# Optimization experiments

Measured on AMD Instinct MI355X. Metric: run time of the kernel, lower is better.

The kernel has to match this reference:

```python
import jax, jax.numpy as jnp
import numpy as np

B, S, E = 256, 512, 1024   # batch, src_len, encoder hidden (== decoder hidden)
H = 1024                   # decoder hidden
AV = 1024                  # att_vec_size
A, TY = 128, 128           # action_embed_size, type_embed_size
T = 48                     # max_sketch_num (decode steps)
NP_, NT_ = 97, 20          # len(prod2id), len(type2id)
IN = A + AV + TY           # LSTMCell input dim = 1280


def setup_inputs() -> dict:
    key = jax.random.key(0)
    ks = jax.random.split(key, 16)
    s = 0.02
    return {
        "encoder_outputs": jax.random.normal(ks[0], (B, S, E), jnp.float32),
        "action_ids": jax.random.randint(ks[1], (T, B), 0, NP_, jnp.int32),
        "type_ids": jax.random.randint(ks[2], (T, B), 0, NT_, jnp.int32),
        "W_ih": jax.random.normal(ks[3], (4 * H, IN), jnp.float32) * s,
        "b_ih": jax.random.normal(ks[4], (4 * H,), jnp.float32) * s,
        "W_hh": jax.random.normal(ks[5], (4 * H, H), jnp.float32) * s,
        "b_hh": jax.random.normal(ks[6], (4 * H,), jnp.float32) * s,
        "W_att": jax.random.normal(ks[7], (H, E), jnp.float32) * s,
        "W_av": jax.random.normal(ks[8], (AV, 2 * H), jnp.float32) * s,
        "W_qa": jax.random.normal(ks[9], (A, AV), jnp.float32) * s,
        "b_qa": jax.random.normal(ks[10], (A,), jnp.float32) * s,
        "prod_embed": jax.random.normal(ks[11], (NP_, A), jnp.float32) * s,
        "prod_bias": jnp.zeros((NP_,), jnp.float32),
        "type_embed_tab": jax.random.normal(ks[12], (NT_, TY), jnp.float32) * s,
        "W_init": jax.random.normal(ks[13], (H, E), jnp.float32) * s,
        "b_init": jax.random.normal(ks[14], (H,), jnp.float32) * s,
    }


def reference(encoder_outputs, action_ids, type_ids, W_ih, b_ih, W_hh, b_hh,
              W_att, W_av, W_qa, b_qa, prod_embed, prod_bias, type_embed_tab,
              W_init, b_init):
    # dropout in eval mode -> identity; src_encodings == encoder_outputs
    src = encoder_outputs                              # [B,S,E]
    src_lin = jnp.einsum('bse,he->bsh', src, W_att)    # att_sketch_linear (no bias)

    # init_decoder_state: adaptive_max_pool1d over sequence, tanh(linear), c0 = 0
    pooled = src.max(axis=1)                           # [B,E]
    h0 = jnp.tanh(pooled @ W_init.T + b_init)          # [B,H]
    c0 = jnp.zeros_like(h0)
    att0 = jnp.zeros((src.shape[0], W_av.shape[0]), src.dtype)

    # previous-action / previous-type embeddings; step 0 uses all-zero input x
    a_prev = prod_embed[action_ids]                    # [T,B,A]
    ty_prev = type_embed_tab[type_ids]                 # [T,B,TY]
    m = (jnp.arange(a_prev.shape[0]) > 0).astype(src.dtype)[:, None, None]  # [T,1,1]
    a_prev = a_prev * m
    ty_prev = ty_prev * m

    def step(carry, xs):
        h, c, att_tm1 = carry
        a_e, ty_e, mt = xs
        x = jnp.concatenate([a_e, att_tm1 * mt, ty_e], axis=-1)  # [B,IN]
        # PyTorch LSTMCell gate order: i, f, g, o
        gates = x @ W_ih.T + b_ih + h @ W_hh.T + b_hh            # [B,4H]
        i, f, g, o = jnp.split(gates, 4, axis=-1)
        c_t = jax.nn.sigmoid(f) * c + jax.nn.sigmoid(i) * jnp.tanh(g)
        h_t = jax.nn.sigmoid(o) * jnp.tanh(c_t)
        # dot-product attention over projected utterance encodings
        scores = jnp.einsum('bsh,bh->bs', src_lin, h_t)
        w = jax.nn.softmax(scores, axis=-1)
        ctx = jnp.einsum('bs,bse->be', w, src)
        att_t = jnp.tanh(jnp.concatenate([h_t, ctx], axis=-1) @ W_av.T)  # [B,AV]
        # production_readout: tanh(linear) then tied production-embedding output layer
        q = jnp.tanh(att_t @ W_qa.T + b_qa)                      # [B,A]
        probs = jax.nn.softmax(q @ prod_embed.T + prod_bias, axis=-1)  # [B,NP]
        return (h_t, c_t, att_t), probs

    _, probs = jax.lax.scan(step, (h0, c0, att0), (a_prev, ty_prev, m))
    return probs  # [T,B,n_prods]
```

## Files before the change

kernel.cpp:

```cpp
#include <hip/hip_runtime.h>


typedef short s16x8 __attribute__((ext_vector_type(8)));
typedef float f32x4 __attribute__((ext_vector_type(4)));

__device__ __forceinline__ unsigned short f2b(float x) {
  unsigned int u = __float_as_uint(x);
  return (unsigned short)((u + 0x7fffu + ((u >> 16) & 1u)) >> 16);
}
__device__ __forceinline__ float b2f(unsigned short h) {
  return __uint_as_float(((unsigned int)h) << 16);
}
__device__ __forceinline__ float sigm(float x) { return 1.f / (1.f + __expf(-x)); }


template <int WRITE_B16>
__global__ __launch_bounds__(256) void pool_convert(const float* __restrict__ src,
                                                    unsigned short* __restrict__ srcb,
                                                    unsigned short* __restrict__ pooledb) {
  int b = blockIdx.x >> 2;
  int e = (blockIdx.x & 3) * 256 + threadIdx.x;
  const float* p = src + (size_t)b * 524288 + e;
  float m = -3e38f;
  for (int s = 0; s < 512; s += 8) {
    float v[8];
#pragma unroll
    for (int i = 0; i < 8; ++i) v[i] = __builtin_nontemporal_load(p + (size_t)(s + i) * 1024);
#pragma unroll
    for (int i = 0; i < 8; ++i) {
      m = fmaxf(m, v[i]);
      if (WRITE_B16) srcb[(size_t)b * 524288 + (size_t)(s + i) * 1024 + e] = f2b(v[i]);
    }
  }
  pooledb[b * 1024 + e] = f2b(m);
}

__global__ __launch_bounds__(256) void conv_wcat(const float* __restrict__ wih,
                                                 const float* __restrict__ whh,
                                                 unsigned short* __restrict__ wcat) {
  int idx = blockIdx.x * 256 + threadIdx.x;
  int np = idx / 2304;
  int k = idx - np * 2304;
  int j = np >> 2, g = np & 3;
  int n = g * 1024 + j;
  float v;
  if (k < 1024) v = wih[n * 1280 + 128 + k];
  else if (k < 2048) v = whh[n * 1024 + (k - 1024)];
  else if (k < 2176) v = wih[n * 1280 + (k - 2048)];
  else v = wih[n * 1280 + 1152 + (k - 2176)];
  wcat[idx] = f2b(v);
}

__global__ __launch_bounds__(256) void conv_bsum(const float* __restrict__ bih,
                                                 const float* __restrict__ bhh,
                                                 float* __restrict__ bsum) {
  int idx = blockIdx.x * 256 + threadIdx.x;
  int j = idx >> 2, g = idx & 3;
  int n = g * 1024 + j;
  bsum[idx] = bih[n] + bhh[n];
}

__global__ __launch_bounds__(256) void conv_wattT(const float* __restrict__ watt,
                                                  unsigned short* __restrict__ wt) {
  int idx = blockIdx.x * 256 + threadIdx.x;
  int e = idx >> 10, h = idx & 1023;
  wt[idx] = f2b(watt[h * 1024 + e]);
}

__global__ __launch_bounds__(256) void conv_f2b(const float* __restrict__ s,
                                                unsigned short* __restrict__ d, int n) {
  int idx = blockIdx.x * 256 + threadIdx.x;
  if (idx < n) d[idx] = f2b(s[idx]);
}

__global__ __launch_bounds__(256) void conv_wqaT(const float* __restrict__ wqa,
                                                 float* __restrict__ wt) {
  int idx = blockIdx.x * 256 + threadIdx.x;
  int k = idx >> 7, j = idx & 127;
  wt[idx] = wqa[j * 1024 + k];
}

__global__ __launch_bounds__(256) void conv_xaty(const int* __restrict__ action,
                                                 const int* __restrict__ type_ids,
                                                 const float* __restrict__ prod_emb,
                                                 const float* __restrict__ type_emb,
                                                 unsigned short* __restrict__ xaty) {
  int idx = blockIdx.x * 256 + threadIdx.x;
  int t = idx >> 16;
  int b = (idx >> 8) & 255;
  int kk = idx & 255;
  float v = 0.f;
  if (t > 0) {
    if (kk < 128) v = prod_emb[action[t * 256 + b] * 128 + kk];
    else v = type_emb[type_ids[t * 256 + b] * 128 + (kk - 128)];
  }
  xaty[idx] = f2b(v);
}

__global__ __launch_bounds__(256) void init0(unsigned short* __restrict__ xs0,
                                             float* __restrict__ c) {
  int idx = blockIdx.x * 256 + threadIdx.x;
  int b = idx >> 10, e = idx & 1023;
  xs0[(size_t)b * 2048 + e] = 0;
  c[idx] = 0.f;
}

template <int EPI, int K>
__global__ __launch_bounds__(256) void gemm_bt(const unsigned short* __restrict__ A, int lda,
                                               const unsigned short* __restrict__ B, int ldb,
                                               float* __restrict__ C, int ldc,
                                               const float* __restrict__ bias,
                                               unsigned short* __restrict__ aux, int aux_ld,
                                               int aux_off) {
  int lane = threadIdx.x & 63;
  int wid = threadIdx.x >> 6;
  int mw = blockIdx.y * 64 + (wid >> 1) * 32;
  int nw = blockIdx.x * 64 + (wid & 1) * 32;
  int lr = lane & 15;
  int kg = lane >> 4;
  const unsigned short* a0p = A + (size_t)(mw + lr) * lda + kg * 8;
  const unsigned short* a1p = a0p + (size_t)16 * lda;
  const unsigned short* b0p = B + (size_t)(nw + lr) * ldb + kg * 8;
  const unsigned short* b1p = b0p + (size_t)16 * ldb;
  f32x4 acc00 = {0.f, 0.f, 0.f, 0.f};
  f32x4 acc01 = acc00, acc10 = acc00, acc11 = acc00;
#pragma unroll 4
  for (int k = 0; k < K; k += 32) {
    s16x8 a0 = *(const s16x8*)(a0p + k);
    s16x8 a1 = *(const s16x8*)(a1p + k);
    s16x8 b0 = *(const s16x8*)(b0p + k);
    s16x8 b1 = *(const s16x8*)(b1p + k);
    acc00 = __builtin_amdgcn_mfma_f32_16x16x32_bf16(a0, b0, acc00, 0, 0, 0);
    acc01 = __builtin_amdgcn_mfma_f32_16x16x32_bf16(a0, b1, acc01, 0, 0, 0);
    acc10 = __builtin_amdgcn_mfma_f32_16x16x32_bf16(a1, b0, acc10, 0, 0, 0);
    acc11 = __builtin_amdgcn_mfma_f32_16x16x32_bf16(a1, b1, acc11, 0, 0, 0);
  }
  int r0 = mw + kg * 4;
  int c0 = nw + lr;
#pragma unroll
  for (int fi = 0; fi < 2; ++fi) {
#pragma unroll
    for (int fj = 0; fj < 2; ++fj) {
      f32x4 acc = (fi == 0) ? (fj == 0 ? acc00 : acc01) : (fj == 0 ? acc10 : acc11);
      int rr = r0 + fi * 16;
      int cc = c0 + fj * 16;
#pragma unroll
      for (int r = 0; r < 4; ++r) {
        float v = acc[r];
        if constexpr (EPI == 2) v = tanhf(v + bias[cc]);
        if constexpr (EPI == 1) v = tanhf(v);
        if constexpr (EPI != 0) aux[(size_t)(rr + r) * aux_ld + aux_off + cc] = f2b(v);
        if constexpr (EPI != 2) C[(size_t)(rr + r) * ldc + cc] = v;
      }
    }
  }
}

template <int EPI, int K>
__global__ __launch_bounds__(256) void gemm32(const unsigned short* __restrict__ A, int lda,
                                              const unsigned short* __restrict__ B, int ldb,
                                              float* __restrict__ C, int ldc,
                                              unsigned short* __restrict__ aux, int aux_ld,
                                              int aux_off) {
  int lane = threadIdx.x & 63;
  int wid = threadIdx.x >> 6;
  int mw = blockIdx.y * 32 + (wid >> 1) * 16;
  int nw = blockIdx.x * 32 + (wid & 1) * 16;
  int lr = lane & 15;
  int kg = lane >> 4;
  const unsigned short* ap = A + (size_t)(mw + lr) * lda + kg * 8;
  const unsigned short* bp = B + (size_t)(nw + lr) * ldb + kg * 8;
  f32x4 acc = {0.f, 0.f, 0.f, 0.f};
#pragma unroll 8
  for (int k = 0; k < K; k += 32) {
    s16x8 a = *(const s16x8*)(ap + k);
    s16x8 b = *(const s16x8*)(bp + k);
    acc = __builtin_amdgcn_mfma_f32_16x16x32_bf16(a, b, acc, 0, 0, 0);
  }
  int rr = mw + kg * 4;
  int cc = nw + lr;
#pragma unroll
  for (int r = 0; r < 4; ++r) {
    float v = acc[r];
    if constexpr (EPI == 1) {
      v = tanhf(v);
      aux[(size_t)(rr + r) * aux_ld + aux_off + cc] = f2b(v);
    }
    C[(size_t)(rr + r) * ldc + cc] = v;
  }
}

__global__ __launch_bounds__(256) void gates_fused(const unsigned short* __restrict__ xin,
                                                   const unsigned short* __restrict__ xaty,
                                                   const unsigned short* __restrict__ wcat,
                                                   const float* __restrict__ bsum,
                                                   float* __restrict__ cbuf,
                                                   unsigned short* __restrict__ xout,
                                                   unsigned short* __restrict__ a2,
                                                   const float* __restrict__ attf,
                                                   const float* __restrict__ wqaT,
                                                   const float* __restrict__ b_qa,
                                                   const float* __restrict__ prod_emb,
                                                   const float* __restrict__ prod_bias,
                                                   float* __restrict__ out, int t) {
  __shared__ float ld[64][68];
  __shared__ float s_att[2][1024];
  __shared__ float s_q2[2][128];
  __shared__ float s_log[2][100];
  __shared__ float s_red[2][2];

  if (blockIdx.y == 4) {
    if (t == 0) return;
    int half = threadIdx.x >> 7;
    int ltid = threadIdx.x & 127;
#pragma unroll
    for (int rep = 0; rep < 2; ++rep) {
      int b = blockIdx.x * 4 + rep * 2 + half;
      const float* ap = attf + (size_t)b * 1024;
      for (int i = ltid; i < 1024; i += 128) s_att[half][i] = ap[i];
      __syncthreads();
      float acc = b_qa[ltid];
      for (int k = 0; k < 1024; ++k) acc += s_att[half][k] * wqaT[k * 128 + ltid];
      s_q2[half][ltid] = tanhf(acc);
      __syncthreads();
      if (ltid < 97) {
        float a = prod_bias[ltid];
        const float* pe = prod_emb + ltid * 128;
        float aa = 0.f;
        for (int k = 0; k < 128; ++k) aa += s_q2[half][k] * pe[k];
        s_log[half][ltid] = a + aa;
      }
      __syncthreads();
      if (ltid == 0) {
        float M = s_log[half][0];
        for (int k2 = 1; k2 < 97; ++k2) M = fmaxf(M, s_log[half][k2]);
        float D = 0.f;
        for (int k2 = 0; k2 < 97; ++k2) D += __expf(s_log[half][k2] - M);
        s_red[half][0] = M;
        s_red[half][1] = D;
      }
      __syncthreads();
      if (ltid < 97)
        out[((size_t)(t - 1) * 256 + b) * 97 + ltid] =
            __expf(s_log[half][ltid] - s_red[half][0]) / s_red[half][1];
      __syncthreads();
    }
    return;
  }

  int lane = threadIdx.x & 63;
  int wid = threadIdx.x >> 6;
  int mwl = (wid >> 1) * 32;
  int nwl = (wid & 1) * 32;
  int mw = blockIdx.y * 64 + mwl;
  int nw = blockIdx.x * 64 + nwl;
  int lr = lane & 15;
  int kg = lane >> 4;
  const unsigned short* a0p = xin + (size_t)(mw + lr) * 2048 + kg * 8;
  const unsigned short* a1p = a0p + (size_t)16 * 2048;
  const unsigned short* b0p = wcat + (size_t)(nw + lr) * 2304 + kg * 8;
  const unsigned short* b1p = b0p + (size_t)16 * 2304;
  f32x4 acc00 = {0.f, 0.f, 0.f, 0.f};
  f32x4 acc01 = acc00, acc10 = acc00, acc11 = acc00;
#pragma unroll 8
  for (int k = 0; k < 2048; k += 32) {
    s16x8 a0 = *(const s16x8*)(a0p + k);
    s16x8 a1 = *(const s16x8*)(a1p + k);
    s16x8 b0 = *(const s16x8*)(b0p + k);
    s16x8 b1 = *(const s16x8*)(b1p + k);
    acc00 = __builtin_amdgcn_mfma_f32_16x16x32_bf16(a0, b0, acc00, 0, 0, 0);
    acc01 = __builtin_amdgcn_mfma_f32_16x16x32_bf16(a0, b1, acc01, 0, 0, 0);
    acc10 = __builtin_amdgcn_mfma_f32_16x16x32_bf16(a1, b0, acc10, 0, 0, 0);
    acc11 = __builtin_amdgcn_mfma_f32_16x16x32_bf16(a1, b1, acc11, 0, 0, 0);
  }
  const unsigned short* c0p = xaty + (size_t)(mw + lr) * 256 + kg * 8;
  const unsigned short* c1p = c0p + (size_t)16 * 256;
#pragma unroll
  for (int k = 0; k < 256; k += 32) {
    s16x8 a0 = *(const s16x8*)(c0p + k);
    s16x8 a1 = *(const s16x8*)(c1p + k);
    s16x8 b0 = *(const s16x8*)(b0p + 2048 + k);
    s16x8 b1 = *(const s16x8*)(b1p + 2048 + k);
    acc00 = __builtin_amdgcn_mfma_f32_16x16x32_bf16(a0, b0, acc00, 0, 0, 0);
    acc01 = __builtin_amdgcn_mfma_f32_16x16x32_bf16(a0, b1, acc01, 0, 0, 0);
    acc10 = __builtin_amdgcn_mfma_f32_16x16x32_bf16(a1, b0, acc10, 0, 0, 0);
    acc11 = __builtin_amdgcn_mfma_f32_16x16x32_bf16(a1, b1, acc11, 0, 0, 0);
  }
  int r0 = mwl + kg * 4;
  int c0 = nwl + lr;
#pragma unroll
  for (int fi = 0; fi < 2; ++fi)
#pragma unroll
    for (int fj = 0; fj < 2; ++fj) {
      f32x4 acc = (fi == 0) ? (fj == 0 ? acc00 : acc01) : (fj == 0 ? acc10 : acc11);
#pragma unroll
      for (int r = 0; r < 4; ++r) ld[r0 + fi * 16 + r][c0 + fj * 16] = acc[r];
    }
  __syncthreads();
  int row = threadIdx.x >> 2;
  int col0 = (threadIdx.x & 3) * 16;
  int b = blockIdx.y * 64 + row;
  int jbase = blockIdx.x * 16 + (threadIdx.x & 3) * 4;
  float4 cold = *(const float4*)(cbuf + (size_t)b * 1024 + jbase);
  float cn[4];
  unsigned short hb[4];
#pragma unroll
  for (int i = 0; i < 4; ++i) {
    float4 bs = *(const float4*)(bsum + (size_t)(jbase + i) * 4);
    float vi = ld[row][col0 + 4 * i + 0] + bs.x;
    float vf = ld[row][col0 + 4 * i + 1] + bs.y;
    float vg = ld[row][col0 + 4 * i + 2] + bs.z;
    float vo = ld[row][col0 + 4 * i + 3] + bs.w;
    float co = (i == 0) ? cold.x : (i == 1) ? cold.y : (i == 2) ? cold.z : cold.w;
    float ct = sigm(vf) * co + sigm(vi) * tanhf(vg);
    float ht = sigm(vo) * tanhf(ct);
    cn[i] = ct;
    hb[i] = f2b(ht);
  }
  *(float4*)(cbuf + (size_t)b * 1024 + jbase) = make_float4(cn[0], cn[1], cn[2], cn[3]);
  ushort4 h4 = make_ushort4(hb[0], hb[1], hb[2], hb[3]);
  *(ushort4*)(xout + (size_t)b * 2048 + 1024 + jbase) = h4;
  *(ushort4*)(a2 + (size_t)b * 2048 + jbase) = h4;
}

template <int BF16P>
__global__ __launch_bounds__(1024) void flash_attn(const unsigned short* __restrict__ srcb,
                                                   const float* __restrict__ srcf,
                                                   const float* __restrict__ q,
                                                   unsigned short* __restrict__ a2) {
  __shared__ unsigned short lctx[16][1024];
  __shared__ float lm[16], ldn[16], lsc[16];
  __shared__ float sDinv;
  int b = blockIdx.x;
  int wid = threadIdx.x >> 6, lane = threadIdx.x & 63;
  float qr[16];
  {
    const float4* qp = (const float4*)(q + (size_t)b * 1024 + lane * 16);
#pragma unroll
    for (int i = 0; i < 4; ++i) {
      float4 t = qp[i];
      qr[4 * i] = t.x; qr[4 * i + 1] = t.y; qr[4 * i + 2] = t.z; qr[4 * i + 3] = t.w;
    }
  }
  float m = -3e38f, d = 0.f;
  float ctx[16];
#pragma unroll
  for (int i = 0; i < 16; ++i) ctx[i] = 0.f;
  int s0 = wid * 32;

  if (BF16P) {
    const unsigned short* rb = srcb + (size_t)b * 524288 + lane * 16;
    s16x8 u0 = __builtin_nontemporal_load((const s16x8*)(rb + (size_t)s0 * 1024));
    s16x8 u1 = __builtin_nontemporal_load((const s16x8*)(rb + (size_t)s0 * 1024 + 8));
    for (int s = 0; s < 32; ++s) {
      int rn = s0 + s + 1;
      rn = rn > 511 ? 511 : rn;
      s16x8 n0 = __builtin_nontemporal_load((const s16x8*)(rb + (size_t)rn * 1024));
      s16x8 n1 = __builtin_nontemporal_load((const s16x8*)(rb + (size_t)rn * 1024 + 8));
      float v[16];
#pragma unroll
      for (int i = 0; i < 8; ++i) {
        v[i] = b2f((unsigned short)u0[i]);
        v[8 + i] = b2f((unsigned short)u1[i]);
      }
      float sc = 0.f;
#pragma unroll
      for (int i = 0; i < 16; ++i) sc += v[i] * qr[i];
#pragma unroll
      for (int off = 1; off < 64; off <<= 1) sc += __shfl_xor(sc, off);
      float mn = fmaxf(m, sc);
      float scale = __expf(m - mn);
      float wgt = __expf(sc - mn);
      d = d * scale + wgt;
#pragma unroll
      for (int i = 0; i < 16; ++i) ctx[i] = ctx[i] * scale + wgt * v[i];
      m = mn;
      u0 = n0; u1 = n1;
    }
  } else {
    const float* rb = srcf + (size_t)b * 524288 + lane * 16;
    for (int s = 0; s < 32; ++s) {
      int r = s0 + s;
      float v[16];
#pragma unroll
      for (int i = 0; i < 4; ++i) {
        f32x4 t = __builtin_nontemporal_load((const f32x4*)(rb + (size_t)r * 1024 + 4 * i));
        v[4 * i] = t[0]; v[4 * i + 1] = t[1]; v[4 * i + 2] = t[2]; v[4 * i + 3] = t[3];
      }
      float sc = 0.f;
#pragma unroll
      for (int i = 0; i < 16; ++i) sc += v[i] * qr[i];
#pragma unroll
      for (int off = 1; off < 64; off <<= 1) sc += __shfl_xor(sc, off);
      float mn = fmaxf(m, sc);
      float scale = __expf(m - mn);
      float wgt = __expf(sc - mn);
      d = d * scale + wgt;
#pragma unroll
      for (int i = 0; i < 16; ++i) ctx[i] = ctx[i] * scale + wgt * v[i];
      m = mn;
    }
  }

#pragma unroll
  for (int i = 0; i < 16; ++i) lctx[wid][lane * 16 + i] = f2b(ctx[i]);
  if (lane == 0) { lm[wid] = m; ldn[wid] = d; }
  __syncthreads();
  if (threadIdx.x == 0) {
    float M = lm[0];
    for (int w2 = 1; w2 < 16; ++w2) M = fmaxf(M, lm[w2]);
    float D = 0.f;
    for (int w2 = 0; w2 < 16; ++w2) {
      float sc = __expf(lm[w2] - M);
      lsc[w2] = sc;
      D += sc * ldn[w2];
    }
    sDinv = 1.f / D;
  }
  __syncthreads();
  int e = threadIdx.x;
  float acc = 0.f;
#pragma unroll
  for (int w2 = 0; w2 < 16; ++w2) acc += lsc[w2] * b2f(lctx[w2][e]);
  a2[(size_t)b * 2048 + 1024 + e] = f2b(acc * sDinv);
}

__global__ __launch_bounds__(128) void readout(const float* __restrict__ att,
                                               const float* __restrict__ wqaT,
                                               const float* __restrict__ b_qa,
                                               const float* __restrict__ prod_emb,
                                               const float* __restrict__ prod_bias,
                                               float* __restrict__ out, int t) {
  __shared__ float s_att[1024], s_q2[128], s_log[97], s_red[2];
  int b = blockIdx.x;
  int tid = threadIdx.x;
  for (int i = tid; i < 1024; i += 128) s_att[i] = att[(size_t)b * 1024 + i];
  __syncthreads();
  float acc = b_qa[tid];
  for (int k = 0; k < 1024; ++k) acc += s_att[k] * wqaT[k * 128 + tid];
  s_q2[tid] = tanhf(acc);
  __syncthreads();
  if (tid < 97) {
    float a = prod_bias[tid];
    const float* pe = prod_emb + tid * 128;
    for (int k = 0; k < 128; ++k) a += s_q2[k] * pe[k];
    s_log[tid] = a;
  }
  __syncthreads();
  if (tid == 0) {
    float M = s_log[0];
    for (int k = 1; k < 97; ++k) M = fmaxf(M, s_log[k]);
    float D = 0.f;
    for (int k = 0; k < 97; ++k) D += __expf(s_log[k] - M);
    s_red[0] = M;
    s_red[1] = D;
  }
  __syncthreads();
  if (tid < 97)
    out[((size_t)t * 256 + b) * 97 + tid] = __expf(s_log[tid] - s_red[0]) / s_red[1];
}


extern "C" void kernel_launch(void* const* d_in, const int* in_sizes, int n_in,
                              void* d_out, int out_size, void* d_ws, size_t ws_size,
                              hipStream_t stream) {
  const float* src = (const float*)d_in[0];
  const int* action = (const int*)d_in[1];
  const int* type_ids = (const int*)d_in[2];
  const float* W_ih = (const float*)d_in[3];
  const float* b_ih = (const float*)d_in[4];
  const float* W_hh = (const float*)d_in[5];
  const float* b_hh = (const float*)d_in[6];
  const float* W_att = (const float*)d_in[7];
  const float* W_av = (const float*)d_in[8];
  const float* W_qa = (const float*)d_in[9];
  const float* b_qa = (const float*)d_in[10];
  const float* prod_emb = (const float*)d_in[11];
  const float* prod_bias = (const float*)d_in[12];
  const float* type_emb = (const float*)d_in[13];
  const float* W_init = (const float*)d_in[14];
  const float* b_init = (const float*)d_in[15];
  float* out = (float*)d_out;

  const size_t NEED_SMALL = 40910848ull;
  const size_t NEED_BIG = 309346304ull;
  bool big = ws_size >= NEED_BIG;
  if (!big && ws_size < NEED_SMALL) return;

  char* w = (char*)d_ws;
  size_t o = 0;
  unsigned short* wcat = (unsigned short*)(w + o); o += 18874368ull;
  unsigned short* wattT = (unsigned short*)(w + o); o += 2097152ull;
  unsigned short* wav = (unsigned short*)(w + o); o += 4194304ull;
  float* wqaT = (float*)(w + o); o += 524288ull;
  unsigned short* xaty = (unsigned short*)(w + o); o += 6291456ull;
  unsigned short* xstate0 = (unsigned short*)(w + o); o += 1048576ull;
  unsigned short* xstate1 = (unsigned short*)(w + o); o += 1048576ull;
  unsigned short* a2 = (unsigned short*)(w + o); o += 1048576ull;
  float* cbuf = (float*)(w + o); o += 1048576ull;
  float* qbuf = (float*)(w + o); o += 1048576ull;
  float* attf = (float*)(w + o); o += 1048576ull;
  unsigned short* pooledb = (unsigned short*)(w + o); o += 524288ull;
  unsigned short* winitb = (unsigned short*)(w + o); o += 2097152ull;
  float* bsum = (float*)(w + o); o += 16384ull;
  unsigned short* srcb = nullptr;
  if (big) { srcb = (unsigned short*)(w + o); o += 268435456ull; }

  if (big) pool_convert<1><<<1024, 256, 0, stream>>>(src, srcb, pooledb);
  else     pool_convert<0><<<1024, 256, 0, stream>>>(src, nullptr, pooledb);
  conv_wcat<<<36864, 256, 0, stream>>>(W_ih, W_hh, wcat);
  conv_bsum<<<16, 256, 0, stream>>>(b_ih, b_hh, bsum);
  conv_wattT<<<4096, 256, 0, stream>>>(W_att, wattT);
  conv_f2b<<<8192, 256, 0, stream>>>(W_av, wav, 2097152);
  conv_f2b<<<4096, 256, 0, stream>>>(W_init, winitb, 1048576);
  conv_wqaT<<<512, 256, 0, stream>>>(W_qa, wqaT);
  conv_xaty<<<12288, 256, 0, stream>>>(action, type_ids, prod_emb, type_emb, xaty);
  init0<<<1024, 256, 0, stream>>>(xstate0, cbuf);
  gemm_bt<2, 1024><<<dim3(16, 4), 256, 0, stream>>>(pooledb, 1024, winitb, 1024,
                                                    nullptr, 0, b_init, xstate0, 2048, 1024);

  for (int t = 0; t < 48; ++t) {
    const unsigned short* xin = (t & 1) ? xstate1 : xstate0;
    unsigned short* xout = (t & 1) ? xstate0 : xstate1;
    gates_fused<<<dim3(64, 5), 256, 0, stream>>>(xin, xaty + (size_t)t * 65536, wcat, bsum,
                                                 cbuf, xout, a2, attf, wqaT, b_qa, prod_emb,
                                                 prod_bias, out, t);
    gemm32<0, 1024><<<dim3(32, 8), 256, 0, stream>>>(a2, 2048, wattT, 1024, qbuf, 1024,
                                                     nullptr, 0, 0);
    if (big) flash_attn<1><<<256, 1024, 0, stream>>>(srcb, nullptr, qbuf, a2);
    else     flash_attn<0><<<256, 1024, 0, stream>>>(nullptr, src, qbuf, a2);
    gemm32<1, 2048><<<dim3(32, 8), 256, 0, stream>>>(a2, 2048, wav, 2048, attf, 1024,
                                                     xout, 2048, 0);
  }
  readout<<<256, 128, 0, stream>>>(attf, wqaT, b_qa, prod_emb, prod_bias, out, 47);
}
```

Before: 6.821 ms.

## Fuse query projection into flash attention and keep half of bf16 src cache-resident

Folds the per-step h·W_att query projection into the attention kernel, so each block computes its own 1024-wide query from h and the transposed W_att. This removes one GEMM launch and the qbuf round trip. The attention block shrinks to 512 threads, each wave streaming 64 rows. The first half of the bf16 source rows is now written and read with normal (temporal) accesses so it can stay in the MI355X's large last-level cache across the 48 steps, while the second half stays non-temporal. The cost is that every one of the 256 blocks re-reads the full 2 MB W_att with a scalar per-thread dot product, and there are fewer waves to hide latency.

```diff
diff --git a/kernel.cpp b/kernel.cpp
--- a/kernel.cpp
+++ b/kernel.cpp
@@ -12,6 +12,17 @@
   return __uint_as_float(((unsigned int)h) << 16);
 }
 __device__ __forceinline__ float sigm(float x) { return 1.f / (1.f + __expf(-x)); }
+
+template <int NT>
+__device__ __forceinline__ s16x8 ld8(const s16x8* p) {
+  if constexpr (NT) return __builtin_nontemporal_load(p);
+  else return *p;
+}
+template <int NT>
+__device__ __forceinline__ f32x4 ld4f(const f32x4* p) {
+  if constexpr (NT) return __builtin_nontemporal_load(p);
+  else return *p;
+}
 
 
 template <int WRITE_B16>
@@ -29,7 +40,12 @@
 #pragma unroll
     for (int i = 0; i < 8; ++i) {
       m = fmaxf(m, v[i]);
-      if (WRITE_B16) srcb[(size_t)b * 524288 + (size_t)(s + i) * 1024 + e] = f2b(v[i]);
+      if (WRITE_B16) {
+        unsigned short bv = f2b(v[i]);
+        unsigned short* dst = srcb + (size_t)b * 524288 + (size_t)(s + i) * 1024 + e;
+        if (s + i < 256) *dst = bv;
+        else __builtin_nontemporal_store(bv, dst);
+      }
     }
   }
   pooledb[b * 1024 + e] = f2b(m);
@@ -323,106 +339,148 @@
   *(ushort4*)(a2 + (size_t)b * 2048 + jbase) = h4;
 }
 
+template <int NT>
+__device__ __forceinline__ void stream_bf16(const unsigned short* rb, int s0,
+                                            const float* qr, float& m, float& d,
+                                            float* ctx) {
+  s16x8 c0 = ld8<NT>((const s16x8*)(rb + (size_t)s0 * 1024));
+  s16x8 c1 = ld8<NT>((const s16x8*)(rb + (size_t)s0 * 1024 + 8));
+  s16x8 d0 = ld8<NT>((const s16x8*)(rb + (size_t)(s0 + 1) * 1024));
+  s16x8 d1 = ld8<NT>((const s16x8*)(rb + (size_t)(s0 + 1) * 1024 + 8));
+  for (int s = 0; s < 64; ++s) {
+    int rn = s0 + s + 2;
+    rn = rn > 511 ? 511 : rn;
+    s16x8 e0 = ld8<NT>((const s16x8*)(rb + (size_t)rn * 1024));
+    s16x8 e1 = ld8<NT>((const s16x8*)(rb + (size_t)rn * 1024 + 8));
+    float v[16];
+#pragma unroll
+    for (int i = 0; i < 8; ++i) {
+      v[i] = b2f((unsigned short)c0[i]);
+      v[8 + i] = b2f((unsigned short)c1[i]);
+    }
+    float sc = 0.f;
+#pragma unroll
+    for (int i = 0; i < 16; ++i) sc += v[i] * qr[i];
+#pragma unroll
+    for (int off = 1; off < 64; off <<= 1) sc += __shfl_xor(sc, off);
+    float mn = fmaxf(m, sc);
+    float scale = __expf(m - mn);
+    float wgt = __expf(sc - mn);
+    d = d * scale + wgt;
+#pragma unroll
+    for (int i = 0; i < 16; ++i) ctx[i] = ctx[i] * scale + wgt * v[i];
+    m = mn;
+    c0 = d0; c1 = d1; d0 = e0; d1 = e1;
+  }
+}
+
+template <int NT>
+__device__ __forceinline__ void stream_f32(const float* rf, int s0, const float* qr,
+                                           float& m, float& d, float* ctx) {
+  for (int s = 0; s < 64; ++s) {
+    int rr = s0 + s;
+    float v[16];
+#pragma unroll
+    for (int i = 0; i < 4; ++i) {
+      f32x4 tq = ld4f<NT>((const f32x4*)(rf + (size_t)rr * 1024 + 4 * i));
+      v[4 * i] = tq[0]; v[4 * i + 1] = tq[1]; v[4 * i + 2] = tq[2]; v[4 * i + 3] = tq[3];
+    }
+    float sc = 0.f;
+#pragma unroll
+    for (int i = 0; i < 16; ++i) sc += v[i] * qr[i];
+#pragma unroll
+    for (int off = 1; off < 64; off <<= 1) sc += __shfl_xor(sc, off);
+    float mn = fmaxf(m, sc);
+    float scale = __expf(m - mn);
+    float wgt = __expf(sc - mn);
+    d = d * scale + wgt;
+#pragma unroll
+    for (int i = 0; i < 16; ++i) ctx[i] = ctx[i] * scale + wgt * v[i];
+    m = mn;
+  }
+}
+
 template <int BF16P>
-__global__ __launch_bounds__(1024) void flash_attn(const unsigned short* __restrict__ srcb,
-                                                   const float* __restrict__ srcf,
-                                                   const float* __restrict__ q,
-                                                   unsigned short* __restrict__ a2) {
-  __shared__ unsigned short lctx[16][1024];
-  __shared__ float lm[16], ldn[16], lsc[16];
-  __shared__ float sDinv;
-  int b = blockIdx.x;
-  int wid = threadIdx.x >> 6, lane = threadIdx.x & 63;
+__global__ __launch_bounds__(512) void flashq(const unsigned short* __restrict__ srcb,
+                                              const float* __restrict__ srcf,
+                                              const unsigned short* __restrict__ wattT,
+                                              unsigned short* __restrict__ a2) {
+  union SMem {
+    struct { float q[1024]; unsigned short h[1024]; } p;
+    struct { unsigned short lctx[8][1024]; float lm[8], ldn[8], lsc[8], sDinv; } c;
+  };
+  __shared__ SMem sm;
+  const int tid = threadIdx.x;
+  const int lane = tid & 63;
+  const int wv = tid >> 6;
+  const int b = blockIdx.x;
+  const int s0 = wv * 64;
+
+  sm.p.h[tid] = a2[(size_t)b * 2048 + tid];
+  sm.p.h[tid + 512] = a2[(size_t)b * 2048 + tid + 512];
+  __syncthreads();
+  {
+    const unsigned short* w0 = wattT + (size_t)(2 * tid) * 1024;
+    const unsigned short* w1 = w0 + 1024;
+    float acc0 = 0.f, acc1 = 0.f;
+    for (int k = 0; k < 1024; k += 8) {
+      s16x8 hv = *(const s16x8*)(sm.p.h + k);
+      s16x8 wa = *(const s16x8*)(w0 + k);
+      s16x8 wb = *(const s16x8*)(w1 + k);
+#pragma unroll
+      for (int i = 0; i < 8; ++i) {
+        float hf = b2f((unsigned short)hv[i]);
+        acc0 += hf * b2f((unsigned short)wa[i]);
+        acc1 += hf * b2f((unsigned short)wb[i]);
+      }
+    }
+    sm.p.q[2 * tid] = acc0;
+    sm.p.q[2 * tid + 1] = acc1;
+  }
+  __syncthreads();
   float qr[16];
-  {
-    const float4* qp = (const float4*)(q + (size_t)b * 1024 + lane * 16);
-#pragma unroll
-    for (int i = 0; i < 4; ++i) {
-      float4 t = qp[i];
-      qr[4 * i] = t.x; qr[4 * i + 1] = t.y; qr[4 * i + 2] = t.z; qr[4 * i + 3] = t.w;
-    }
-  }
+#pragma unroll
+  for (int i = 0; i < 16; ++i) qr[i] = sm.p.q[lane * 16 + i];
+  __syncthreads();
+
   float m = -3e38f, d = 0.f;
   float ctx[16];
 #pragma unroll
   for (int i = 0; i < 16; ++i) ctx[i] = 0.f;
-  int s0 = wid * 32;
-
   if (BF16P) {
     const unsigned short* rb = srcb + (size_t)b * 524288 + lane * 16;
-    s16x8 u0 = __builtin_nontemporal_load((const s16x8*)(rb + (size_t)s0 * 1024));
-    s16x8 u1 = __builtin_nontemporal_load((const s16x8*)(rb + (size_t)s0 * 1024 + 8));
-    for (int s = 0; s < 32; ++s) {
-      int rn = s0 + s + 1;
-      rn = rn > 511 ? 511 : rn;
-      s16x8 n0 = __builtin_nontemporal_load((const s16x8*)(rb + (size_t)rn * 1024));
-      s16x8 n1 = __builtin_nontemporal_load((const s16x8*)(rb + (size_t)rn * 1024 + 8));
-      float v[16];
-#pragma unroll
-      for (int i = 0; i < 8; ++i) {
-        v[i] = b2f((unsigned short)u0[i]);
-        v[8 + i] = b2f((unsigned short)u1[i]);
-      }
-      float sc = 0.f;
-#pragma unroll
-      for (int i = 0; i < 16; ++i) sc += v[i] * qr[i];
-#pragma unroll
-      for (int off = 1; off < 64; off <<= 1) sc += __shfl_xor(sc, off);
-      float mn = fmaxf(m, sc);
-      float scale = __expf(m - mn);
-      float wgt = __expf(sc - mn);
-      d = d * scale + wgt;
-#pragma unroll
-      for (int i = 0; i < 16; ++i) ctx[i] = ctx[i] * scale + wgt * v[i];
-      m = mn;
-      u0 = n0; u1 = n1;
-    }
+    if (wv < 4) stream_bf16<0>(rb, s0, qr, m, d, ctx);
+    else        stream_bf16<1>(rb, s0, qr, m, d, ctx);
   } else {
-    const float* rb = srcf + (size_t)b * 524288 + lane * 16;
-    for (int s = 0; s < 32; ++s) {
-      int r = s0 + s;
-      float v[16];
-#pragma unroll
-      for (int i = 0; i < 4; ++i) {
-        f32x4 t = __builtin_nontemporal_load((const f32x4*)(rb + (size_t)r * 1024 + 4 * i));
-        v[4 * i] = t[0]; v[4 * i + 1] = t[1]; v[4 * i + 2] = t[2]; v[4 * i + 3] = t[3];
-      }
-      float sc = 0.f;
-#pragma unroll
-      for (int i = 0; i < 16; ++i) sc += v[i] * qr[i];
-#pragma unroll
-      for (int off = 1; off < 64; off <<= 1) sc += __shfl_xor(sc, off);
-      float mn = fmaxf(m, sc);
-      float scale = __expf(m - mn);
-      float wgt = __expf(sc - mn);
-      d = d * scale + wgt;
-#pragma unroll
-      for (int i = 0; i < 16; ++i) ctx[i] = ctx[i] * scale + wgt * v[i];
-      m = mn;
-    }
-  }
-
-#pragma unroll
-  for (int i = 0; i < 16; ++i) lctx[wid][lane * 16 + i] = f2b(ctx[i]);
-  if (lane == 0) { lm[wid] = m; ldn[wid] = d; }
-  __syncthreads();
-  if (threadIdx.x == 0) {
-    float M = lm[0];
-    for (int w2 = 1; w2 < 16; ++w2) M = fmaxf(M, lm[w2]);
+    const float* rf = srcf + (size_t)b * 524288 + lane * 16;
+    if (wv < 4) stream_f32<0>(rf, s0, qr, m, d, ctx);
+    else        stream_f32<1>(rf, s0, qr, m, d, ctx);
+  }
+
+#pragma unroll
+  for (int i = 0; i < 16; ++i) sm.c.lctx[wv][lane * 16 + i] = f2b(ctx[i]);
+  if (lane == 0) { sm.c.lm[wv] = m; sm.c.ldn[wv] = d; }
+  __syncthreads();
+  if (tid == 0) {
+    float M = sm.c.lm[0];
+    for (int w2 = 1; w2 < 8; ++w2) M = fmaxf(M, sm.c.lm[w2]);
     float D = 0.f;
-    for (int w2 = 0; w2 < 16; ++w2) {
-      float sc = __expf(lm[w2] - M);
-      lsc[w2] = sc;
-      D += sc * ldn[w2];
-    }
-    sDinv = 1.f / D;
-  }
-  __syncthreads();
-  int e = threadIdx.x;
-  float acc = 0.f;
-#pragma unroll
-  for (int w2 = 0; w2 < 16; ++w2) acc += lsc[w2] * b2f(lctx[w2][e]);
-  a2[(size_t)b * 2048 + 1024 + e] = f2b(acc * sDinv);
+    for (int w2 = 0; w2 < 8; ++w2) {
+      float sc = __expf(sm.c.lm[w2] - M);
+      sm.c.lsc[w2] = sc;
+      D += sc * sm.c.ldn[w2];
+    }
+    sm.c.sDinv = 1.f / D;
+  }
+  __syncthreads();
+#pragma unroll
+  for (int half = 0; half < 2; ++half) {
+    int e = tid + half * 512;
+    float acc2 = 0.f;
+#pragma unroll
+    for (int w2 = 0; w2 < 8; ++w2) acc2 += sm.c.lsc[w2] * b2f(sm.c.lctx[w2][e]);
+    a2[(size_t)b * 2048 + 1024 + e] = f2b(acc2 * sm.c.sDinv);
+  }
 }
 
 __global__ __launch_bounds__(128) void readout(const float* __restrict__ att,
@@ -482,8 +540,8 @@
   const float* b_init = (const float*)d_in[15];
   float* out = (float*)d_out;
 
-  const size_t NEED_SMALL = 40910848ull;
-  const size_t NEED_BIG = 309346304ull;
+  const size_t NEED_SMALL = 39862272ull;
+  const size_t NEED_BIG = 308297728ull;
   bool big = ws_size >= NEED_BIG;
   if (!big && ws_size < NEED_SMALL) return;
 
@@ -498,7 +556,6 @@
   unsigned short* xstate1 = (unsigned short*)(w + o); o += 1048576ull;
   unsigned short* a2 = (unsigned short*)(w + o); o += 1048576ull;
   float* cbuf = (float*)(w + o); o += 1048576ull;
-  float* qbuf = (float*)(w + o); o += 1048576ull;
   float* attf = (float*)(w + o); o += 1048576ull;
   unsigned short* pooledb = (unsigned short*)(w + o); o += 524288ull;
   unsigned short* winitb = (unsigned short*)(w + o); o += 2097152ull;
@@ -525,10 +582,8 @@
     gates_fused<<<dim3(64, 5), 256, 0, stream>>>(xin, xaty + (size_t)t * 65536, wcat, bsum,
                                                  cbuf, xout, a2, attf, wqaT, b_qa, prod_emb,
                                                  prod_bias, out, t);
-    gemm32<0, 1024><<<dim3(32, 8), 256, 0, stream>>>(a2, 2048, wattT, 1024, qbuf, 1024,
-                                                     nullptr, 0, 0);
-    if (big) flash_attn<1><<<256, 1024, 0, stream>>>(srcb, nullptr, qbuf, a2);
-    else     flash_attn<0><<<256, 1024, 0, stream>>>(nullptr, src, qbuf, a2);
+    if (big) flashq<1><<<256, 512, 0, stream>>>(srcb, nullptr, wattT, a2);
+    else     flashq<0><<<256, 512, 0, stream>>>(nullptr, src, wattT, a2);
     gemm32<1, 2048><<<dim3(32, 8), 256, 0, stream>>>(a2, 2048, wav, 2048, attf, 1024,
                                                      xout, 2048, 0);
   }
```

Result: slower. 10.63 ms (+55.8%).
